# Performance work log

Measured on AMD Instinct MI355X. Metric: run time of the kernel, lower is better.

Reference implementation:

```python
import math
import jax, jax.numpy as jnp
import numpy as np

B, C, H, W, R, P = 4, 64, 128, 128, 5, 8


def circular_sample(x, r):
    """Bilinear ring sampling, grid_sample(align_corners=True, padding_mode='zeros') equivalent.
    x: [B,C,H,W]; returns [B,H,W,C,P]."""
    Bx, Cx, Hx, Wx = x.shape
    angles = jnp.linspace(0.0, 2.0 * math.pi, P + 1)[:-1]
    di = r * jnp.sin(angles)  # row offsets [P]
    dj = r * jnp.cos(angles)  # col offsets [P]
    yy = jnp.arange(Hx, dtype=x.dtype)[:, None, None] + di[None, None, :]  # [H,1,P]
    xx = jnp.arange(Wx, dtype=x.dtype)[None, :, None] + dj[None, None, :]  # [1,W,P]
    yy = jnp.broadcast_to(yy, (Hx, Wx, P))
    xx = jnp.broadcast_to(xx, (Hx, Wx, P))
    y0 = jnp.floor(yy); x0 = jnp.floor(xx)
    wy = yy - y0; wx = xx - x0
    y0i = y0.astype(jnp.int32); x0i = x0.astype(jnp.int32)

    def gather(yi, xi):
        valid = ((yi >= 0) & (yi < Hx) & (xi >= 0) & (xi < Wx)).astype(x.dtype)
        yc = jnp.clip(yi, 0, Hx - 1)
        xc = jnp.clip(xi, 0, Wx - 1)
        return x[:, :, yc, xc] * valid  # [B,C,H,W,P], zeros padding

    v00 = gather(y0i, x0i)
    v01 = gather(y0i, x0i + 1)
    v10 = gather(y0i + 1, x0i)
    v11 = gather(y0i + 1, x0i + 1)
    out = (v00 * (1 - wy) * (1 - wx) + v01 * (1 - wy) * wx
           + v10 * wy * (1 - wx) + v11 * wy * wx)
    return jnp.transpose(out, (0, 2, 3, 1, 4))  # [B,H,W,C,P] -> channel-major, point-minor


def setup_inputs() -> dict:
    key = jax.random.key(0)
    ks = jax.random.split(key, 3)
    x = jax.random.normal(ks[0], (B, C, H, W), dtype=jnp.float32)
    CP = C * P
    W1 = jax.random.normal(ks[1], (R, CP, 64), dtype=jnp.float32) / np.sqrt(CP)
    b1 = jnp.zeros((R, 64), dtype=jnp.float32)
    g1 = jnp.ones((R, 64), dtype=jnp.float32)
    bt1 = jnp.zeros((R, 64), dtype=jnp.float32)
    W2 = jax.random.normal(ks[2], (R, 64, C), dtype=jnp.float32) / 8.0
    b2 = jnp.zeros((R, C), dtype=jnp.float32)
    return {"x": x, "W1": W1, "b1": b1, "g1": g1, "bt1": bt1, "W2": W2, "b2": b2}


def reference(x, W1, b1, g1, bt1, W2, b2):
    Bx, Cx, Hx, Wx = x.shape
    acc = jnp.zeros((Bx, Hx * Wx, Cx), dtype=x.dtype)
    for r in range(R):  # small fixed radius loop, matches module structure
        feat = circular_sample(x, float(r)).reshape(Bx, Hx * Wx, Cx * P)
        h = feat @ W1[r] + b1[r]
        mu = jnp.mean(h, axis=-1, keepdims=True)
        var = jnp.mean((h - mu) ** 2, axis=-1, keepdims=True)
        h = (h - mu) / jnp.sqrt(var + 1e-5) * g1[r] + bt1[r]
        h = jax.nn.gelu(h, approximate=False)  # torch nn.GELU default = exact erf
        acc = acc + h @ W2[r] + b2[r]
    wts = jax.nn.sigmoid(acc).reshape(Bx, Hx, Wx, Cx).transpose(0, 3, 1, 2)
    return x * wts
```

## Files before the change

### kernel.cpp

```cpp
#include <hip/hip_runtime.h>
#include <math.h>

namespace {
constexpr int Hh = 128, Ww = 128;
constexpr int NDCAP = 48;
constexpr int UROW  = 56;

using short8 = __attribute__((ext_vector_type(8))) short;
using f32x4  = __attribute__((ext_vector_type(4))) float;

__device__ __forceinline__ unsigned short f2bf(float f) {
    union { float f; unsigned int u; } v; v.f = f;
    unsigned int u = v.u;
    unsigned int r = (u + 0x7FFFu + ((u >> 16) & 1u)) >> 16;
    return (unsigned short)r;
}

constexpr size_t XBF_OFF  = 0;
constexpr size_t W1P_OFF  = 8388608;
constexpr size_t W2P_OFF  = W1P_OFF + (size_t)484 * 4096;
constexpr size_t META_OFF = W2P_OFF + 40960;
constexpr size_t UOFF_OFF = META_OFF + 64;
constexpr size_t WVEC_OFF = UOFF_OFF + 1152;
constexpr size_t WS_NEED  = WVEC_OFF + 7680;
}

__global__ void rrf_table(int* __restrict__ meta, int* __restrict__ uoff,
                          float* __restrict__ wvec)
{
    __shared__ float grid[5][81][8];
    __shared__ unsigned char keep[5][81];
    __shared__ short dofs[5][81];
    __shared__ int nds[5];

    const int t = threadIdx.x;
    for (int i = t; i < 5 * 81 * 8; i += 512) ((float*)grid)[i] = 0.f;
    for (int i = t; i < 5 * UROW; i += 512) uoff[i] = 0;
    __syncthreads();

    if (t < 40) {
        int r = t >> 3, p = t & 7;
        float ang = (float)p * 0.78539818525314331f;
        float si = (float)sin((double)ang);
        float co = (float)cos((double)ang);
        float di = (float)r * si;
        float dj = (float)r * co;
        float y0f = floorf(di), x0f = floorf(dj);
        float wy = di - y0f, wx = dj - x0f;
        int y0 = (int)y0f, x0 = (int)x0f;
        float tw[4] = {(1.f - wy) * (1.f - wx), (1.f - wy) * wx,
                       wy * (1.f - wx), wy * wx};
        int ty[4] = {y0, y0, y0 + 1, y0 + 1};
        int tx[4] = {x0, x0 + 1, x0, x0 + 1};
        #pragma unroll
        for (int q = 0; q < 4; ++q) {
            if (fabsf(tw[q]) < 1e-6f) continue;
            grid[r][(ty[q] + 4) * 9 + (tx[q] + 4)][p] = tw[q];
        }
    }
    __syncthreads();

    if (t < 405) {
        int r = t / 81, ci = t - r * 81;
        float mx = 0.f;
        #pragma unroll
        for (int p = 0; p < 8; ++p) mx = fmaxf(mx, fabsf(grid[r][ci][p]));
        keep[r][ci] = (mx > 1e-6f) ? 1 : 0;
    }
    __syncthreads();

    if (t < 5) {
        int nd = 0;
        for (int ci = 0; ci < 81; ++ci) {
            dofs[t][ci] = (short)nd;
            nd += keep[t][ci];
        }
        nds[t] = nd;
    }
    __syncthreads();

    if (t < 405) {
        int r = t / 81, ci = t - r * 81;
        if (keep[r][ci]) {
            int d = dofs[r][ci];
            int iy = ci / 9, ix = ci - iy * 9;
            uoff[r * UROW + d] = (iy * 24 + (ix - 4)) * 80;
            #pragma unroll
            for (int p = 0; p < 8; ++p)
                wvec[(r * NDCAP + d) * 8 + p] = grid[r][ci][p];
        }
    }
    if (t == 0) {
        int base = 0;
        for (int r = 0; r < 5; ++r) {
            int nd  = nds[r];
            int ndp = (nd + 3) & ~3;
            meta[r]      = ndp;
            meta[5 + r]  = base;
            meta[11 + r] = nd;
            base += ndp;
        }
        meta[10] = base;
    }
}

__global__ void rrf_pack(const float* __restrict__ W1, const float* __restrict__ W2,
                         const int* __restrict__ meta, const float* __restrict__ wvec,
                         unsigned short* __restrict__ w1p, unsigned short* __restrict__ w2p)
{
    int bb = blockIdx.x;
    if (bb < 480) {
        int gid  = bb * 256 + threadIdx.x;
        int lane = gid & 63;
        int t    = (gid >> 6) & 3;
        int cc   = (gid >> 8) & 1;
        int rd   = gid >> 9;
        int r = rd / NDCAP, d = rd % NDCAP;
        if (r >= 5 || d >= meta[r]) return;
        int TOTP  = meta[10];
        int chunk = cc * TOTP + meta[5 + r] + d;
        unsigned short* dst = w1p + ((size_t)(chunk * 4 + t) * 64 + lane) * 8;
        if (d >= meta[11 + r]) {
            short8 z = {0,0,0,0,0,0,0,0};
            *(short8*)dst = z;
            return;
        }
        int n = t * 16 + (lane & 15);
        int cbase = cc * 32 + ((lane >> 4) << 3);
        const float* wv  = wvec + (r * NDCAP + d) * 8;
        const float* w1r = W1 + (size_t)r * 512 * 64;
        short8 o;
        #pragma unroll
        for (int j = 0; j < 8; ++j) {
            int c = cbase + j;
            float acc = 0.f;
            #pragma unroll
            for (int p = 0; p < 8; ++p)
                acc = fmaf(wv[p], w1r[(c * 8 + p) * 64 + n], acc);
            o[j] = (short)f2bf(acc);
        }
        *(short8*)dst = o;
    } else {
        int i = (bb - 480) * 256 + threadIdx.x;
        if (i < 20480) {
            int j    = i & 7;
            int lane = (i >> 3) & 63;
            int kc2  = (i >> 9) & 1;
            int t    = (i >> 10) & 3;
            int r    = i >> 12;
            int n = kc2 * 32 + ((lane >> 4) << 3) + j;
            int m = t * 16 + (lane & 15);
            w2p[i] = f2bf(W2[(r * 64 + n) * 64 + m]);
        }
    }
}

__global__ void rrf_xpose(const float* __restrict__ x, unsigned short* __restrict__ xbf)
{
    __shared__ float tl[64][65];
    int b   = blockIdx.x >> 8;
    int px0 = (blockIdx.x & 255) * 64;
    int tx = threadIdx.x & 63, ty = threadIdx.x >> 6;
    #pragma unroll
    for (int i = 0; i < 16; ++i) {
        int c = i * 4 + ty;
        tl[c][tx] = x[(((size_t)b * 64 + c) << 14) + px0 + tx];
    }
    __syncthreads();
    #pragma unroll
    for (int i = 0; i < 16; ++i) {
        int px = i * 4 + ty;
        xbf[(((size_t)b << 14) + px0 + px) * 64 + tx] = f2bf(tl[tx][px]);
    }
}

#define LDA4(K, CI) { const unsigned short* _q = ap + (size_t)(CI) * 2048 + tpoff + (lane << 3); \
    A##K[0] = *(const short8*)(_q); A##K[1] = *(const short8*)(_q + 512); }

#define LDB4(K, U) {                                                                      \
    B##K[0] = *(const short8*)(tb + ((U) + lb0));                                         \
    B##K[1] = *(const short8*)(tb + ((U) + lb1));                                         \
    B##K[2] = *(const short8*)(tb + ((U) + lb2));                                         \
    B##K[3] = *(const short8*)(tb + ((U) + lb3)); }

#define MF4(K) {                                                                          \
    _Pragma("unroll")                                                                     \
    for (int _q = 0; _q < 4; ++_q) {                                                      \
        hv[0][_q] = __builtin_amdgcn_mfma_f32_16x16x32_bf16(A##K[0], B##K[_q], hv[0][_q], 0, 0, 0); \
        hv[1][_q] = __builtin_amdgcn_mfma_f32_16x16x32_bf16(A##K[1], B##K[_q], hv[1][_q], 0, 0, 0); \
    } }

__global__ __launch_bounds__(512, 2)
void rrf_stencil4(const float* __restrict__ x, const unsigned short* __restrict__ xbf,
                  const unsigned short* __restrict__ w1p, const unsigned short* __restrict__ w2p,
                  const int* __restrict__ meta, const int* __restrict__ uoff,
                  const float* __restrict__ b1v, const float* __restrict__ g1v,
                  const float* __restrict__ btv, const float* __restrict__ b2v,
                  float* __restrict__ out)
{
    __shared__ __align__(16) unsigned short tile[2][23040];
    __shared__ __align__(16) unsigned short gbuf[16][16][72];
    __shared__ float wsum[2][4][4][16][2];
    __shared__ int uo_lds[5 * UROW];
    __shared__ int meta_lds[16];

    const int tid  = threadIdx.x;
    const int w    = tid >> 6;
    const int lane = tid & 63;
    const int col  = lane & 15;
    const int g    = lane >> 4;
    const int tp   = w & 1;
    const int rq   = w >> 1;
    const int tpoff = tp * 1024;

    const int bid = blockIdx.x;
    const int b   = bid >> 6;
    const int r0  = ((bid >> 3) & 7) * 16;
    const int c0  = (bid & 7) * 16;

    const int lb0 = ((4 * rq + 0) * 24 + col + 4) * 80 + g * 16;
    const int lb1 = ((4 * rq + 1) * 24 + col + 4) * 80 + g * 16;
    const int lb2 = ((4 * rq + 2) * 24 + col + 4) * 80 + g * 16;
    const int lb3 = ((4 * rq + 3) * 24 + col + 4) * 80 + g * 16;

    for (int s = tid; s < 5 * UROW; s += 512) uo_lds[s] = uoff[s];
    if (tid < 16) meta_lds[tid] = meta[tid];

    for (int s = tid; s < 576; s += 512) {
        int trow = s / 24, tcol = s - trow * 24;
        int row = r0 - 4 + trow, cg = c0 - 4 + tcol;
        bool valid = ((unsigned)row < 128u) && ((unsigned)cg < 128u);
        unsigned short* d0 = &tile[0][s * 40];
        unsigned short* d1 = &tile[1][s * 40];
        if (valid) {
            const unsigned short* src =
                xbf + (((size_t)(b << 14)) + row * 128 + cg) * 64;
            #pragma unroll
            for (int k = 0; k < 4; ++k) {
                *(short8*)(d0 + k * 8) = *(const short8*)(src + k * 8);
                *(short8*)(d1 + k * 8) = *(const short8*)(src + 32 + k * 8);
            }
        } else {
            short8 z = {0, 0, 0, 0, 0, 0, 0, 0};
            #pragma unroll
            for (int k = 0; k < 4; ++k) {
                *(short8*)(d0 + k * 8) = z;
                *(short8*)(d1 + k * 8) = z;
            }
        }
    }
    __syncthreads();

    f32x4 acc2[4][4];
    #pragma unroll
    for (int t = 0; t < 4; ++t)
        #pragma unroll
        for (int q = 0; q < 4; ++q) acc2[t][q] = f32x4{0.f, 0.f, 0.f, 0.f};

    #pragma unroll 1
    for (int r = 0; r < 5; ++r) {
        f32x4 hv[2][4];
        #pragma unroll
        for (int t = 0; t < 2; ++t)
            #pragma unroll
            for (int q = 0; q < 4; ++q) hv[t][q] = f32x4{0.f, 0.f, 0.f, 0.f};

        const int ndp  = __builtin_amdgcn_readfirstlane(meta_lds[r]);
        const int base = __builtin_amdgcn_readfirstlane(meta_lds[5 + r]);
        const int TOTP = __builtin_amdgcn_readfirstlane(meta_lds[10]);
        const int* uo = uo_lds + r * UROW;

        #pragma unroll 1
        for (int cc = 0; cc < 2; ++cc) {
            const unsigned short* ap = w1p + (size_t)(cc * TOTP + base) * 2048;
            const char* tb = (const char*)(&tile[cc][0]);

            short8 A0[2], A1[2], A2[2], A3[2];
            short8 B0[4], B1[4], B2[4], B3[4];
            LDA4(0, 0) LDB4(0, uo[0])
            LDA4(1, 1) LDB4(1, uo[1])
            LDA4(2, 2) LDB4(2, uo[2])
            LDA4(3, 3) LDB4(3, uo[3])
            int u0 = uo[4], u1 = uo[5], u2 = uo[6], u3 = uo[7];
            #pragma unroll 1
            for (int d = 0; d < ndp; d += 4) {
                MF4(0) LDA4(0, d + 4) LDB4(0, u0)
                MF4(1) LDA4(1, d + 5) LDB4(1, u1)
                MF4(2) LDA4(2, d + 6) LDB4(2, u2)
                MF4(3) LDA4(3, d + 7) LDB4(3, u3)
                u0 = uo[d + 8];  u1 = uo[d + 9];
                u2 = uo[d + 10]; u3 = uo[d + 11];
            }
        }

        float b1r[2][4], g1r[2][4], btr[2][4];
        #pragma unroll
        for (int t = 0; t < 2; ++t)
            #pragma unroll
            for (int e = 0; e < 4; ++e) {
                int n = (2 * tp + t) * 16 + g * 4 + e;
                b1r[t][e] = b1v[r * 64 + n];
                g1r[t][e] = g1v[r * 64 + n];
                btr[t][e] = btv[r * 64 + n];
            }

        float hq[2][4][4];
        float sA[4], sB[4];
        #pragma unroll
        for (int q = 0; q < 4; ++q) {
            float s = 0.f, s2 = 0.f;
            #pragma unroll
            for (int t = 0; t < 2; ++t)
                #pragma unroll
                for (int e = 0; e < 4; ++e) {
                    float v = hv[t][q][e] + b1r[t][e];
                    hq[t][q][e] = v;
                    s += v;
                    s2 = fmaf(v, v, s2);
                }
            s  += __shfl_xor(s, 16);  s  += __shfl_xor(s, 32);
            s2 += __shfl_xor(s2, 16); s2 += __shfl_xor(s2, 32);
            sA[q] = s; sB[q] = s2;
        }
        if (g == 0) {
            #pragma unroll
            for (int q = 0; q < 4; ++q) {
                wsum[tp][rq][q][col][0] = sA[q];
                wsum[tp][rq][q][col][1] = sB[q];
            }
        }
        __syncthreads();

        #pragma unroll
        for (int q = 0; q < 4; ++q) {
            float so  = wsum[tp ^ 1][rq][q][col][0];
            float s2o = wsum[tp ^ 1][rq][q][col][1];
            const float mu = (sA[q] + so) * 0.015625f;
            const float ms = (sB[q] + s2o) * 0.015625f;
            const float rs = rsqrtf(ms - mu * mu + 1e-5f);
            const int row = 4 * rq + q;
            #pragma unroll
            for (int t = 0; t < 2; ++t) {
                float ge[4];
                #pragma unroll
                for (int e = 0; e < 4; ++e) {
                    float v = (hq[t][q][e] - mu) * rs * g1r[t][e] + btr[t][e];
                    ge[e] = 0.5f * v * (1.f + erff(v * 0.70710678118654752f));
                }
                int n0 = (2 * tp + t) * 16 + g * 4;
                *(unsigned int*)&gbuf[row][col][n0] =
                    (unsigned int)f2bf(ge[0]) | ((unsigned int)f2bf(ge[1]) << 16);
                *(unsigned int*)&gbuf[row][col][n0 + 2] =
                    (unsigned int)f2bf(ge[2]) | ((unsigned int)f2bf(ge[3]) << 16);
            }
        }
        __syncthreads();

        const unsigned short* a2base = w2p + (size_t)r * 4096 + (size_t)lane * 8;
        short8 a2f[2][4];
        #pragma unroll
        for (int kc2 = 0; kc2 < 2; ++kc2)
            #pragma unroll
            for (int t = 0; t < 4; ++t)
                a2f[kc2][t] = *(const short8*)(a2base + kc2 * 512 + t * 1024);

        #pragma unroll
        for (int q = 0; q < 4; ++q) {
            const int row = 4 * rq + q;
            #pragma unroll
            for (int kc2 = 0; kc2 < 2; ++kc2) {
                short8 bf2 = *(const short8*)&gbuf[row][col][kc2 * 32 + g * 8];
                #pragma unroll
                for (int t = 0; t < 4; ++t)
                    acc2[t][q] = __builtin_amdgcn_mfma_f32_16x16x32_bf16(
                        a2f[kc2][t], bf2, acc2[t][q], 0, 0, 0);
            }
        }
    }

    #pragma unroll
    for (int t = 0; t < 4; ++t) {
        #pragma unroll
        for (int e = 0; e < 4; ++e) {
            int m = t * 16 + g * 4 + e;
            float sb = b2v[m] + b2v[64 + m] + b2v[128 + m] + b2v[192 + m] + b2v[256 + m];
            #pragma unroll
            for (int q = 0; q < 4; ++q) {
                float a = acc2[t][q][e] + sb;
                float wts = 1.f / (1.f + expf(-a));
                size_t off = (((size_t)b * 64 + m) << 14)
                           + (size_t)(r0 + 4 * rq + q) * 128 + (c0 + col);
                out[off] = x[off] * wts;
            }
        }
    }
}

__global__ void rrf_prepack(const float* __restrict__ W1, const float* __restrict__ W2,
                            unsigned short* __restrict__ w1p, unsigned short* __restrict__ w2p)
{
    int i = blockIdx.x * 256 + threadIdx.x;
    if (i < 163840) {
        int jq   = i & 7;
        int lane = (i >> 3) & 63;
        int kc   = (i >> 9) & 15;
        int t    = (i >> 13) & 3;
        int r    = i >> 15;
        int k = kc * 32 + ((lane >> 4) << 3) + jq;
        int n = t * 16 + (lane & 15);
        w1p[i] = f2bf(W1[(r * 512 + k) * 64 + n]);
    }
    if (i < 20480) {
        int jq   = i & 7;
        int lane = (i >> 3) & 63;
        int kc2  = (i >> 9) & 1;
        int t    = (i >> 10) & 3;
        int r    = i >> 12;
        int n = kc2 * 32 + ((lane >> 4) << 3) + jq;
        int m = t * 16 + (lane & 15);
        w2p[i] = f2bf(W2[(r * 64 + n) * 64 + m]);
    }
}

__global__ __launch_bounds__(256, 2)
void rrf_mfma(const float* __restrict__ x,
              const unsigned short* __restrict__ w1p, const unsigned short* __restrict__ w2p,
              const float* __restrict__ b1v, const float* __restrict__ g1v,
              const float* __restrict__ btv, const float* __restrict__ b2v,
              float* __restrict__ out)
{
    __shared__ unsigned short gbuf[4][16][72];

    const int tid  = threadIdx.x;
    const int w    = tid >> 6;
    const int lane = tid & 63;
    const int col  = lane & 15;
    const int g    = lane >> 4;

    const int bid  = blockIdx.x;
    const int b    = bid >> 8;
    const int rem  = bid & 255;
    const int irow = rem >> 1;
    const int j0   = (rem & 1) * 64;
    const int j    = j0 + w * 16 + col;

    const float fi = (float)irow;
    const float fj = (float)j;
    const float* xb = x + ((size_t)b << 20);

    f32x4 acc2[4] = {f32x4{0,0,0,0}, f32x4{0,0,0,0}, f32x4{0,0,0,0}, f32x4{0,0,0,0}};

    #pragma unroll 1
    for (int r = 0; r < 5; ++r) {
        int   o00[8], o01[8], o10[8], o11[8];
        float w00[8], w01[8], w10[8], w11[8];
        const float rf = (float)r;
        #pragma unroll
        for (int p = 0; p < 8; ++p) {
            float ang = (float)p * 0.78539818525314331f;
            float yy = fi + rf * sinf(ang);
            float xx = fj + rf * cosf(ang);
            float y0f = floorf(yy), x0f = floorf(xx);
            float wy = yy - y0f, wx = xx - x0f;
            int y0 = (int)y0f, x0i = (int)x0f;
            int y1 = y0 + 1,   x1  = x0i + 1;
            float m00 = (y0 >= 0 && y0 < Hh && x0i >= 0 && x0i < Ww) ? 1.f : 0.f;
            float m01 = (y0 >= 0 && y0 < Hh && x1  >= 0 && x1  < Ww) ? 1.f : 0.f;
            float m10 = (y1 >= 0 && y1 < Hh && x0i >= 0 && x0i < Ww) ? 1.f : 0.f;
            float m11 = (y1 >= 0 && y1 < Hh && x1  >= 0 && x1  < Ww) ? 1.f : 0.f;
            int y0c = y0 < 0 ? 0 : (y0 > Hh - 1 ? Hh - 1 : y0);
            int y1c = y1 < 0 ? 0 : (y1 > Hh - 1 ? Hh - 1 : y1);
            int x0c = x0i < 0 ? 0 : (x0i > Ww - 1 ? Ww - 1 : x0i);
            int x1c = x1 < 0 ? 0 : (x1 > Ww - 1 ? Ww - 1 : x1);
            w00[p] = (1.f - wy) * (1.f - wx) * m00;
            w01[p] = (1.f - wy) * wx * m01;
            w10[p] = wy * (1.f - wx) * m10;
            w11[p] = wy * wx * m11;
            o00[p] = (y0c * Ww + x0c) * 4;
            o01[p] = (y0c * Ww + x1c) * 4;
            o10[p] = (y1c * Ww + x0c) * 4;
            o11[p] = (y1c * Ww + x1c) * 4;
        }

        f32x4 hv[4] = {f32x4{0,0,0,0}, f32x4{0,0,0,0}, f32x4{0,0,0,0}, f32x4{0,0,0,0}};
        const unsigned short* abase0 = w1p + ((size_t)((r * 64) * 64 + lane)) * 8;
        #pragma unroll 2
        for (int kc = 0; kc < 16; ++kc) {
            const int c = (kc << 2) + g;
            const char* xp = (const char*)(xb + ((size_t)c << 14));
            short8 bfrag;
            #pragma unroll
            for (int p = 0; p < 8; ++p) {
                float v00 = *(const float*)(xp + o00[p]);
                float v01 = *(const float*)(xp + o01[p]);
                float v10 = *(const float*)(xp + o10[p]);
                float v11 = *(const float*)(xp + o11[p]);
                float v = w00[p] * v00;
                v = fmaf(w01[p], v01, v);
                v = fmaf(w10[p], v10, v);
                v = fmaf(w11[p], v11, v);
                bfrag[p] = (short)f2bf(v);
            }
            const unsigned short* ab = abase0 + (size_t)kc * 512;
            #pragma unroll
            for (int t = 0; t < 4; ++t) {
                short8 af = *(const short8*)(ab + (size_t)t * 8192);
                hv[t] = __builtin_amdgcn_mfma_f32_16x16x32_bf16(af, bfrag, hv[t], 0, 0, 0);
            }
        }

        const int nb = g << 2;
        float hq[4][4];
        float s = 0.f;
        #pragma unroll
        for (int t = 0; t < 4; ++t)
            #pragma unroll
            for (int q = 0; q < 4; ++q) {
                float hvq = hv[t][q] + b1v[r * 64 + t * 16 + nb + q];
                hq[t][q] = hvq;
                s += hvq;
            }
        s += __shfl_xor(s, 16);
        s += __shfl_xor(s, 32);
        const float mu = s * 0.015625f;
        float s2 = 0.f;
        #pragma unroll
        for (int t = 0; t < 4; ++t)
            #pragma unroll
            for (int q = 0; q < 4; ++q) {
                float d = hq[t][q] - mu;
                s2 = fmaf(d, d, s2);
            }
        s2 += __shfl_xor(s2, 16);
        s2 += __shfl_xor(s2, 32);
        const float rs = rsqrtf(s2 * 0.015625f + 1e-5f);

        #pragma unroll
        for (int t = 0; t < 4; ++t)
            #pragma unroll
            for (int q = 0; q < 4; ++q) {
                int n = t * 16 + nb + q;
                float v = (hq[t][q] - mu) * rs * g1v[r * 64 + n] + btv[r * 64 + n];
                hq[t][q] = 0.5f * v * (1.f + erff(v * 0.70710678118654752f));
            }
        #pragma unroll
        for (int t = 0; t < 4; ++t) {
            #pragma unroll
            for (int q2 = 0; q2 < 4; q2 += 2) {
                unsigned int u = (unsigned int)f2bf(hq[t][q2])
                               | ((unsigned int)f2bf(hq[t][q2 + 1]) << 16);
                *(unsigned int*)&gbuf[w][col][t * 16 + nb + q2] = u;
            }
        }

        const unsigned short* a2base = w2p + ((size_t)((r * 8) * 64 + lane)) * 8;
        #pragma unroll
        for (int kc2 = 0; kc2 < 2; ++kc2) {
            short8 bf2 = *(const short8*)&gbuf[w][col][kc2 * 32 + g * 8];
            const unsigned short* a2 = a2base + (size_t)kc2 * 512;
            #pragma unroll
            for (int t = 0; t < 4; ++t) {
                short8 a2f = *(const short8*)(a2 + (size_t)t * 1024);
                acc2[t] = __builtin_amdgcn_mfma_f32_16x16x32_bf16(a2f, bf2, acc2[t], 0, 0, 0);
            }
        }
    }

    #pragma unroll
    for (int t = 0; t < 4; ++t) {
        #pragma unroll
        for (int q = 0; q < 4; ++q) {
            int m = t * 16 + (g << 2) + q;
            float sb = b2v[m] + b2v[64 + m] + b2v[128 + m] + b2v[192 + m] + b2v[256 + m];
            float a = acc2[t][q] + sb;
            float wts = 1.f / (1.f + expf(-a));
            size_t off = (((size_t)b * 64 + m) << 14) + ((size_t)irow << 7) + j;
            out[off] = x[off] * wts;
        }
    }
}

extern "C" void kernel_launch(void* const* d_in, const int* in_sizes, int n_in,
                              void* d_out, int out_size, void* d_ws, size_t ws_size,
                              hipStream_t stream)
{
    const float* x  = (const float*)d_in[0];
    const float* W1 = (const float*)d_in[1];
    const float* b1 = (const float*)d_in[2];
    const float* g1 = (const float*)d_in[3];
    const float* bt = (const float*)d_in[4];
    const float* W2 = (const float*)d_in[5];
    const float* b2 = (const float*)d_in[6];
    float* outp = (float*)d_out;
    char* ws = (char*)d_ws;

    if (ws_size >= WS_NEED) {
        unsigned short* xbf = (unsigned short*)(ws + XBF_OFF);
        unsigned short* w1p = (unsigned short*)(ws + W1P_OFF);
        unsigned short* w2p = (unsigned short*)(ws + W2P_OFF);
        int*   meta  = (int*)(ws + META_OFF);
        int*   uoffp = (int*)(ws + UOFF_OFF);
        float* wvec  = (float*)(ws + WVEC_OFF);

        rrf_xpose<<<dim3(1024), dim3(256), 0, stream>>>(x, xbf);
        rrf_table<<<dim3(1), dim3(512), 0, stream>>>(meta, uoffp, wvec);
        rrf_pack<<<dim3(564), dim3(256), 0, stream>>>(W1, W2, meta, wvec, w1p, w2p);
        rrf_stencil4<<<dim3(256), dim3(512), 0, stream>>>(x, xbf, w1p, w2p, meta, uoffp,
                                                          b1, g1, bt, b2, outp);
    } else {
        unsigned short* w1p = (unsigned short*)d_ws;
        unsigned short* w2p = w1p + 163840;
        rrf_prepack<<<dim3(640), dim3(256), 0, stream>>>(W1, W2, w1p, w2p);
        rrf_mfma<<<dim3(1024), dim3(256), 0, stream>>>(x, w1p, w2p, b1, g1, bt, b2, outp);
    }
}
```

Measured before the change: 98.65 us.

## Double threads per block in stencil kernel, halving rows per wave

The main stencil kernel now launches 1024 threads (16 waves) per block instead of 512. Each wave owns 2 pixel rows instead of 4, so per-wave accumulators, B-fragment loads and the second GEMM shrink accordingly. The intent is more waves per tile to hide LDS and global latency with fewer registers per thread. In exchange each wave reloads the shared W1/W2 fragments, one block fits per CU, and an extra barrier per radius iteration guards gbuf reuse.

Measured after the change: 97.39 us. No clear change (-1.3%).

```diff
diff --git a/kernel.cpp b/kernel.cpp
--- a/kernel.cpp
+++ b/kernel.cpp
@@ -174,24 +174,21 @@
     }
 }
 
-#define LDA4(K, CI) { const unsigned short* _q = ap + (size_t)(CI) * 2048 + tpoff + (lane << 3); \
+#define LDA6(K, CI) { const unsigned short* _q = ap + (size_t)(CI) * 2048 + tsel + (lane << 3); \
     A##K[0] = *(const short8*)(_q); A##K[1] = *(const short8*)(_q + 512); }
 
-#define LDB4(K, U) {                                                                      \
-    B##K[0] = *(const short8*)(tb + ((U) + lb0));                                         \
-    B##K[1] = *(const short8*)(tb + ((U) + lb1));                                         \
-    B##K[2] = *(const short8*)(tb + ((U) + lb2));                                         \
-    B##K[3] = *(const short8*)(tb + ((U) + lb3)); }
-
-#define MF4(K) {                                                                          \
-    _Pragma("unroll")                                                                     \
-    for (int _q = 0; _q < 4; ++_q) {                                                      \
-        hv[0][_q] = __builtin_amdgcn_mfma_f32_16x16x32_bf16(A##K[0], B##K[_q], hv[0][_q], 0, 0, 0); \
-        hv[1][_q] = __builtin_amdgcn_mfma_f32_16x16x32_bf16(A##K[1], B##K[_q], hv[1][_q], 0, 0, 0); \
-    } }
-
-__global__ __launch_bounds__(512, 2)
-void rrf_stencil4(const float* __restrict__ x, const unsigned short* __restrict__ xbf,
+#define LDB6(K, U) {                                                                      \
+    B##K[0] = *(const short8*)(tb + ((U) + lbq0));                                        \
+    B##K[1] = *(const short8*)(tb + ((U) + lbq1)); }
+
+#define MF6(K) {                                                                          \
+    hv[0][0] = __builtin_amdgcn_mfma_f32_16x16x32_bf16(A##K[0], B##K[0], hv[0][0], 0, 0, 0); \
+    hv[0][1] = __builtin_amdgcn_mfma_f32_16x16x32_bf16(A##K[0], B##K[1], hv[0][1], 0, 0, 0); \
+    hv[1][0] = __builtin_amdgcn_mfma_f32_16x16x32_bf16(A##K[1], B##K[0], hv[1][0], 0, 0, 0); \
+    hv[1][1] = __builtin_amdgcn_mfma_f32_16x16x32_bf16(A##K[1], B##K[1], hv[1][1], 0, 0, 0); }
+
+__global__ __launch_bounds__(1024, 1)
+void rrf_stencil6(const float* __restrict__ x, const unsigned short* __restrict__ xbf,
                   const unsigned short* __restrict__ w1p, const unsigned short* __restrict__ w2p,
                   const int* __restrict__ meta, const int* __restrict__ uoff,
                   const float* __restrict__ b1v, const float* __restrict__ g1v,
@@ -200,7 +197,7 @@
 {
     __shared__ __align__(16) unsigned short tile[2][23040];
     __shared__ __align__(16) unsigned short gbuf[16][16][72];
-    __shared__ float wsum[2][4][4][16][2];
+    __shared__ float wsum[2][8][2][16][2];
     __shared__ int uo_lds[5 * UROW];
     __shared__ int meta_lds[16];
 
@@ -210,23 +207,22 @@
     const int col  = lane & 15;
     const int g    = lane >> 4;
     const int tp   = w & 1;
-    const int rq   = w >> 1;
-    const int tpoff = tp * 1024;
+    const int pg   = w >> 1;
+    const int tsel = tp * 1024;
 
     const int bid = blockIdx.x;
     const int b   = bid >> 6;
     const int r0  = ((bid >> 3) & 7) * 16;
     const int c0  = (bid & 7) * 16;
 
-    const int lb0 = ((4 * rq + 0) * 24 + col + 4) * 80 + g * 16;
-    const int lb1 = ((4 * rq + 1) * 24 + col + 4) * 80 + g * 16;
-    const int lb2 = ((4 * rq + 2) * 24 + col + 4) * 80 + g * 16;
-    const int lb3 = ((4 * rq + 3) * 24 + col + 4) * 80 + g * 16;
-
-    for (int s = tid; s < 5 * UROW; s += 512) uo_lds[s] = uoff[s];
+    const int lbq0 = ((2 * pg + 0) * 24 + col + 4) * 80 + g * 16;
+    const int lbq1 = ((2 * pg + 1) * 24 + col + 4) * 80 + g * 16;
+
+    if (tid < 5 * UROW) uo_lds[tid] = uoff[tid];
     if (tid < 16) meta_lds[tid] = meta[tid];
 
-    for (int s = tid; s < 576; s += 512) {
+    if (tid < 576) {
+        int s = tid;
         int trow = s / 24, tcol = s - trow * 24;
         int row = r0 - 4 + trow, cg = c0 - 4 + tcol;
         bool valid = ((unsigned)row < 128u) && ((unsigned)cg < 128u);
@@ -251,19 +247,17 @@
     }
     __syncthreads();
 
-    f32x4 acc2[4][4];
+    f32x4 acc2[4];
     #pragma unroll
-    for (int t = 0; t < 4; ++t)
-        #pragma unroll
-        for (int q = 0; q < 4; ++q) acc2[t][q] = f32x4{0.f, 0.f, 0.f, 0.f};
+    for (int t = 0; t < 4; ++t) acc2[t] = f32x4{0.f, 0.f, 0.f, 0.f};
 
     #pragma unroll 1
     for (int r = 0; r < 5; ++r) {
-        f32x4 hv[2][4];
+        f32x4 hv[2][2];
         #pragma unroll
         for (int t = 0; t < 2; ++t)
             #pragma unroll
-            for (int q = 0; q < 4; ++q) hv[t][q] = f32x4{0.f, 0.f, 0.f, 0.f};
+            for (int q = 0; q < 2; ++q) hv[t][q] = f32x4{0.f, 0.f, 0.f, 0.f};
 
         const int ndp  = __builtin_amdgcn_readfirstlane(meta_lds[r]);
         const int base = __builtin_amdgcn_readfirstlane(meta_lds[5 + r]);
@@ -276,18 +270,18 @@
             const char* tb = (const char*)(&tile[cc][0]);
 
             short8 A0[2], A1[2], A2[2], A3[2];
-            short8 B0[4], B1[4], B2[4], B3[4];
-            LDA4(0, 0) LDB4(0, uo[0])
-            LDA4(1, 1) LDB4(1, uo[1])
-            LDA4(2, 2) LDB4(2, uo[2])
-            LDA4(3, 3) LDB4(3, uo[3])
+            short8 B0[2], B1[2], B2[2], B3[2];
+            LDA6(0, 0) LDB6(0, uo[0])
+            LDA6(1, 1) LDB6(1, uo[1])
+            LDA6(2, 2) LDB6(2, uo[2])
+            LDA6(3, 3) LDB6(3, uo[3])
             int u0 = uo[4], u1 = uo[5], u2 = uo[6], u3 = uo[7];
             #pragma unroll 1
             for (int d = 0; d < ndp; d += 4) {
-                MF4(0) LDA4(0, d + 4) LDB4(0, u0)
-                MF4(1) LDA4(1, d + 5) LDB4(1, u1)
-                MF4(2) LDA4(2, d + 6) LDB4(2, u2)
-                MF4(3) LDA4(3, d + 7) LDB4(3, u3)
+                MF6(0) LDA6(0, d + 4) LDB6(0, u0)
+                MF6(1) LDA6(1, d + 5) LDB6(1, u1)
+                MF6(2) LDA6(2, d + 6) LDB6(2, u2)
+                MF6(3) LDA6(3, d + 7) LDB6(3, u3)
                 u0 = uo[d + 8];  u1 = uo[d + 9];
                 u2 = uo[d + 10]; u3 = uo[d + 11];
             }
@@ -304,10 +298,10 @@
                 btr[t][e] = btv[r * 64 + n];
             }
 
-        float hq[2][4][4];
-        float sA[4], sB[4];
-        #pragma unroll
-        for (int q = 0; q < 4; ++q) {
+        float hq[2][2][4];
+        float sA[2], sB[2];
+        #pragma unroll
+        for (int q = 0; q < 2; ++q) {
             float s = 0.f, s2 = 0.f;
             #pragma unroll
             for (int t = 0; t < 2; ++t)
@@ -324,21 +318,21 @@
         }
         if (g == 0) {
             #pragma unroll
-            for (int q = 0; q < 4; ++q) {
-                wsum[tp][rq][q][col][0] = sA[q];
-                wsum[tp][rq][q][col][1] = sB[q];
+            for (int q = 0; q < 2; ++q) {
+                wsum[tp][pg][q][col][0] = sA[q];
+                wsum[tp][pg][q][col][1] = sB[q];
             }
         }
         __syncthreads();
 
         #pragma unroll
-        for (int q = 0; q < 4; ++q) {
-            float so  = wsum[tp ^ 1][rq][q][col][0];
-            float s2o = wsum[tp ^ 1][rq][q][col][1];
+        for (int q = 0; q < 2; ++q) {
+            float so  = wsum[tp ^ 1][pg][q][col][0];
+            float s2o = wsum[tp ^ 1][pg][q][col][1];
             const float mu = (sA[q] + so) * 0.015625f;
             const float ms = (sB[q] + s2o) * 0.015625f;
             const float rs = rsqrtf(ms - mu * mu + 1e-5f);
-            const int row = 4 * rq + q;
+            const int row = 2 * pg + q;
             #pragma unroll
             for (int t = 0; t < 2; ++t) {
                 float ge[4];
@@ -357,25 +351,16 @@
         __syncthreads();
 
         const unsigned short* a2base = w2p + (size_t)r * 4096 + (size_t)lane * 8;
-        short8 a2f[2][4];
-        #pragma unroll
-        for (int kc2 = 0; kc2 < 2; ++kc2)
-            #pragma unroll
-            for (int t = 0; t < 4; ++t)
-                a2f[kc2][t] = *(const short8*)(a2base + kc2 * 512 + t * 1024);
-
-        #pragma unroll
-        for (int q = 0; q < 4; ++q) {
-            const int row = 4 * rq + q;
-            #pragma unroll
-            for (int kc2 = 0; kc2 < 2; ++kc2) {
-                short8 bf2 = *(const short8*)&gbuf[row][col][kc2 * 32 + g * 8];
-                #pragma unroll
-                for (int t = 0; t < 4; ++t)
-                    acc2[t][q] = __builtin_amdgcn_mfma_f32_16x16x32_bf16(
-                        a2f[kc2][t], bf2, acc2[t][q], 0, 0, 0);
-            }
-        }
+        #pragma unroll
+        for (int kc2 = 0; kc2 < 2; ++kc2) {
+            short8 bf2 = *(const short8*)&gbuf[w][col][kc2 * 32 + g * 8];
+            #pragma unroll
+            for (int t = 0; t < 4; ++t) {
+                short8 a2f = *(const short8*)(a2base + kc2 * 512 + t * 1024);
+                acc2[t] = __builtin_amdgcn_mfma_f32_16x16x32_bf16(a2f, bf2, acc2[t], 0, 0, 0);
+            }
+        }
+        if (r < 4) __syncthreads();
     }
 
     #pragma unroll
@@ -384,14 +369,11 @@
         for (int e = 0; e < 4; ++e) {
             int m = t * 16 + g * 4 + e;
             float sb = b2v[m] + b2v[64 + m] + b2v[128 + m] + b2v[192 + m] + b2v[256 + m];
-            #pragma unroll
-            for (int q = 0; q < 4; ++q) {
-                float a = acc2[t][q][e] + sb;
-                float wts = 1.f / (1.f + expf(-a));
-                size_t off = (((size_t)b * 64 + m) << 14)
-                           + (size_t)(r0 + 4 * rq + q) * 128 + (c0 + col);
-                out[off] = x[off] * wts;
-            }
+            float a = acc2[t][e] + sb;
+            float wts = 1.f / (1.f + expf(-a));
+            size_t off = (((size_t)b * 64 + m) << 14)
+                       + (size_t)(r0 + w) * 128 + (c0 + col);
+            out[off] = x[off] * wts;
         }
     }
 }
@@ -605,8 +587,8 @@
         rrf_xpose<<<dim3(1024), dim3(256), 0, stream>>>(x, xbf);
         rrf_table<<<dim3(1), dim3(512), 0, stream>>>(meta, uoffp, wvec);
         rrf_pack<<<dim3(564), dim3(256), 0, stream>>>(W1, W2, meta, wvec, w1p, w2p);
-        rrf_stencil4<<<dim3(256), dim3(512), 0, stream>>>(x, xbf, w1p, w2p, meta, uoffp,
-                                                          b1, g1, bt, b2, outp);
+        rrf_stencil6<<<dim3(256), dim3(1024), 0, stream>>>(x, xbf, w1p, w2p, meta, uoffp,
+                                                           b1, g1, bt, b2, outp);
     } else {
         unsigned short* w1p = (unsigned short*)d_ws;
         unsigned short* w2p = w1p + 163840;
```
